# Optimization experiments

Measured on AMD Instinct MI355X. Metric: run time of the kernel, lower is better.

## Reference

```python
import jax, jax.numpy as jnp
import numpy as np

H = 16          # num_heads
K = 15          # kernel_size (padding_l = K-1, causal)
EPS = 1e-5      # LayerNorm eps


def setup_inputs() -> dict:
    key = jax.random.key(0)
    ks = jax.random.split(key, 8)
    T, B, C, F = 1024, 8, 1024, 4096
    n = lambda k, shape, scale=1.0: jax.random.normal(k, shape, jnp.float32) * scale
    return {
        "x": n(ks[0], (T, B, C)),
        "w_lin": n(ks[1], (C, H * K), 0.02),      # dynamic-conv weight projection
        "b_lin": jnp.zeros((H * K,), jnp.float32),
        "ln_g": jnp.ones((C,), jnp.float32),
        "ln_b": jnp.zeros((C,), jnp.float32),
        "fc1_w": n(ks[2], (C, F), 0.02),
        "fc1_b": jnp.zeros((F,), jnp.float32),
        "fc2_w": n(ks[3], (F, C), 0.02),
        "fc2_b": jnp.zeros((C,), jnp.float32),
    }


def _dynamic_conv(x, w_lin, b_lin):
    # x: (T, B, C). Per-timestep weights -> softmax over kernel -> causal conv.
    T, B, C = x.shape
    R = C // H  # channels per head
    w = jnp.einsum('tbc,ck->tbk', x, w_lin) + b_lin          # (T, B, H*K)
    w = jax.nn.softmax(w.reshape(T, B, H, K), axis=-1)        # softmax over kernel taps
    # causal left-padding: tap k sees x[t + k - (K-1)]
    xp = jnp.pad(x, ((K - 1, 0), (0, 0), (0, 0))).reshape(T + K - 1, B, H, R)
    o = jnp.zeros((T, B, H, R), x.dtype)
    for k in range(K):  # fixed small kernel loop; avoids (T,B,C,K) unfold tensor
        o = o + w[:, :, :, k:k + 1] * xp[k:k + T]
    return o.reshape(T, B, C)


def _layer_norm(y, g, b):
    mu = jnp.mean(y, axis=-1, keepdims=True)
    var = jnp.var(y, axis=-1, keepdims=True)
    return (y - mu) * jax.lax.rsqrt(var + EPS) * g + b


def _forward(x, w_lin, b_lin, ln_g, ln_b, fc1_w, fc1_b, fc2_w, fc2_b):
    y = _dynamic_conv(x, w_lin, b_lin)
    y = _layer_norm(y, ln_g, ln_b)
    h = jax.nn.relu(jnp.einsum('tbc,cf->tbf', y, fc1_w) + fc1_b)
    out = jnp.einsum('tbf,fc->tbc', h, fc2_w) + fc2_b
    return out + y  # residual around FFN (residual taken post-LayerNorm)


def reference(x, w_lin, b_lin, ln_g, ln_b, fc1_w, fc1_b, fc2_w, fc2_b):
    return _forward(x, w_lin, b_lin, ln_g, ln_b, fc1_w, fc1_b, fc2_w, fc2_b)
```

## Files before the change

kernel.cpp:

```cpp
#include <hip/hip_runtime.h>


#define T_DIM 1024
#define B_DIM 8
#define C_DIM 1024
#define F_DIM 4096
#define H_DIM 16
#define K_TAP 15
#define TB (T_DIM * B_DIM)

typedef __attribute__((ext_vector_type(8))) short short8;
typedef __attribute__((ext_vector_type(4))) float f32x4;

__device__ __forceinline__ float bf2f(unsigned short u) {
    union { unsigned int i; float f; } v; v.i = ((unsigned int)u) << 16; return v.f;
}
__device__ __forceinline__ unsigned short f2bf(float f) {
    union { float f; unsigned int i; } v; v.f = f;
    unsigned int r = v.i + 0x7fffu + ((v.i >> 16) & 1u);
    return (unsigned short)(r >> 16);
}

__device__ __forceinline__ void async_copy16(const void* gptr, void* lptr) {
    __builtin_amdgcn_global_load_lds(
        (const __attribute__((address_space(1))) void*)gptr,
        (__attribute__((address_space(3))) void*)lptr, 16, 0, 0);
}

__global__ __launch_bounds__(256)
void prep(const float* __restrict__ fc1_w, unsigned short* __restrict__ fc1T,
          const float* __restrict__ fc2_w, unsigned short* __restrict__ fc2T,
          const float* __restrict__ w_lin, unsigned short* __restrict__ wlinT) {
    const int bid = blockIdx.x;
    const int tid = threadIdx.x;
    const float* in; unsigned short* out; int R, Cin, c0, r0;
    if (bid < 1024) {
        int idx = bid;
        in = fc1_w; out = fc1T; R = C_DIM; Cin = F_DIM;
        c0 = (idx & 63) * 64; r0 = (idx >> 6) * 64;
    } else if (bid < 2048) {
        int idx = bid - 1024;
        in = fc2_w; out = fc2T; R = F_DIM; Cin = C_DIM;
        c0 = (idx & 15) * 64; r0 = (idx >> 4) * 64;
    } else {
        int idx = bid - 2048;
        in = w_lin; out = wlinT; R = C_DIM; Cin = 240;
        c0 = (idx & 3) * 64; r0 = (idx >> 2) * 64;
    }
    __shared__ unsigned short tile[64][65];
    const int xx = tid & 63, yy = tid >> 6;
#pragma unroll
    for (int j = 0; j < 16; j++) {
        int r = r0 + yy + j * 4, c = c0 + xx;
        unsigned short v = 0;
        if (c < Cin) v = f2bf(in[(size_t)r * Cin + c]);
        tile[yy + j * 4][xx] = v;
    }
    __syncthreads();
#pragma unroll
    for (int j = 0; j < 16; j++) {
        out[(size_t)(c0 + yy + j * 4) * R + (r0 + xx)] = tile[xx][yy + j * 4];
    }
}

template <int MODE, int SWAP>
__global__ __launch_bounds__(256)
void gemm_bt(const unsigned short* __restrict__ A,
             const unsigned short* __restrict__ Bt,
             void* __restrict__ Cout_v,
             int M, int N, int K, int kz,
             const float* __restrict__ bias,
             const unsigned short* __restrict__ resid) {
    __shared__ __align__(16) unsigned short As[2][128 * 64];
    __shared__ __align__(16) unsigned short Bs[2][128 * 64];

    const int tid = threadIdx.x;
    const int m0 = (SWAP ? blockIdx.x : blockIdx.y) * 128;
    const int n0 = (SWAP ? blockIdx.y : blockIdx.x) * 128;
    const int kbase = blockIdx.z * kz;
    const int wave = tid >> 6, lane = tid & 63;
    const int quad = lane >> 4, l16 = lane & 15;
    const int wm = (wave >> 1) * 64;
    const int wn = (wave & 1) * 64;

    f32x4 acc[4][4];
#pragma unroll
    for (int i = 0; i < 4; i++)
#pragma unroll
        for (int j = 0; j < 4; j++) acc[i][j] = (f32x4){0.f, 0.f, 0.f, 0.f};

    const int rsub = lane >> 3;
    const int gch = (lane & 7) ^ rsub;
    const unsigned short* gA = A + (size_t)(m0 + wave * 32 + rsub) * K + kbase + gch * 8;
    const unsigned short* gB = Bt + (size_t)(n0 + wave * 32 + rsub) * K + kbase + gch * 8;
    unsigned short* lA[2] = {&As[0][wave * 32 * 64], &As[1][wave * 32 * 64]};
    unsigned short* lB[2] = {&Bs[0][wave * 32 * 64], &Bs[1][wave * 32 * 64]};

#pragma unroll
    for (int j = 0; j < 4; j++) {
        async_copy16(gA + (size_t)j * 8 * K, lA[0] + j * 8 * 64);
        async_copy16(gB + (size_t)j * 8 * K, lB[0] + j * 8 * 64);
    }

    const int swz = l16 & 7;
    int buf = 0;
    for (int k0 = 0; k0 < kz; k0 += 64) {
        __syncthreads();

        const int nk = k0 + 64;
        if (nk < kz) {
            const int nb = buf ^ 1;
#pragma unroll
            for (int j = 0; j < 4; j++) {
                async_copy16(gA + nk + (size_t)j * 8 * K, lA[nb] + j * 8 * 64);
                async_copy16(gB + nk + (size_t)j * 8 * K, lB[nb] + j * 8 * 64);
            }
        }

        short8 af[2][4], bfr[2][4];
#pragma unroll
        for (int kk = 0; kk < 2; kk++) {
            const int c = kk * 4 + quad;
#pragma unroll
            for (int i = 0; i < 4; i++) {
                af[kk][i]  = *(const short8*)(&As[buf][(wm + i * 16 + l16) * 64 + (c ^ swz) * 8]);
                bfr[kk][i] = *(const short8*)(&Bs[buf][(wn + i * 16 + l16) * 64 + (c ^ swz) * 8]);
            }
        }
#pragma unroll
        for (int kk = 0; kk < 2; kk++)
#pragma unroll
            for (int mi = 0; mi < 4; mi++)
#pragma unroll
                for (int nj = 0; nj < 4; nj++)
                    acc[mi][nj] = __builtin_amdgcn_mfma_f32_16x16x32_bf16(
                        af[kk][mi], bfr[kk][nj], acc[mi][nj], 0, 0, 0);
        buf ^= 1;
    }

    const int crow0 = m0 + wm + quad * 4;
    const int ccol0 = n0 + wn + l16;
    if (MODE == 1) {
        unsigned short* Cb = (unsigned short*)Cout_v;
        float bv[4];
#pragma unroll
        for (int nj = 0; nj < 4; nj++) bv[nj] = bias[ccol0 + nj * 16];
#pragma unroll
        for (int mi = 0; mi < 4; mi++)
#pragma unroll
            for (int i = 0; i < 4; i++) {
                int rr = crow0 + mi * 16 + i;
#pragma unroll
                for (int nj = 0; nj < 4; nj++) {
                    float v = fmaxf(acc[mi][nj][i] + bv[nj], 0.f);
                    Cb[(size_t)rr * N + ccol0 + nj * 16] = f2bf(v);
                }
            }
    } else {
        float* Cf = (float*)Cout_v;
        float bv[4];
#pragma unroll
        for (int nj = 0; nj < 4; nj++) bv[nj] = bias[ccol0 + nj * 16];
#pragma unroll
        for (int mi = 0; mi < 4; mi++)
#pragma unroll
            for (int i = 0; i < 4; i++) {
                int rr = crow0 + mi * 16 + i;
#pragma unroll
                for (int nj = 0; nj < 4; nj++) {
                    float v = acc[mi][nj][i] + bv[nj]
                            + bf2f(resid[(size_t)rr * N + ccol0 + nj * 16]);
                    Cf[(size_t)rr * N + ccol0 + nj * 16] = v;
                }
            }
    }
}

#define XSP 1032
__global__ __launch_bounds__(256)
void megaconv(const float* __restrict__ x,
              const unsigned short* __restrict__ wlinT,
              const float* __restrict__ b_lin,
              const float* __restrict__ ln_g,
              const float* __restrict__ ln_b,
              unsigned short* __restrict__ y) {
    __shared__ __align__(16) unsigned short xs[30 * XSP];
    __shared__ float wls[16 * 240];
    const int blk = blockIdx.x;
    const int b = blk & 7;
    const int t0 = (blk >> 3) * 16;
    const int tid = threadIdx.x;
    const int wave = tid >> 6, lane = tid & 63;
    const int quad = lane >> 4, l16 = lane & 15;

#pragma unroll
    for (int j = 0; j < 30; j++) {
        const int t = t0 + j - 14;
        uint2 o = make_uint2(0u, 0u);
        if (t >= 0) {
            float4 v = *(const float4*)(x + ((size_t)t * B_DIM + b) * C_DIM + tid * 4);
            o.x = (unsigned int)f2bf(v.x) | ((unsigned int)f2bf(v.y) << 16);
            o.y = (unsigned int)f2bf(v.z) | ((unsigned int)f2bf(v.w) << 16);
        }
        *(uint2*)(&xs[j * XSP + tid * 4]) = o;
    }
    __syncthreads();

    {
        f32x4 lacc[4];
#pragma unroll
        for (int i = 0; i < 4; i++) lacc[i] = (f32x4){0.f, 0.f, 0.f, 0.f};
        const unsigned short* xrow = &xs[(14 + l16) * XSP + quad * 8];
        const unsigned short* brow = wlinT + (size_t)l16 * C_DIM + quad * 8;
#pragma unroll 8
        for (int kk = 0; kk < 32; kk++) {
            short8 af = *(const short8*)(xrow + kk * 32);
#pragma unroll
            for (int j = 0; j < 4; j++) {
                const int nt = wave + j * 4;
                if (nt < 15) {
                    short8 bf = *(const short8*)(brow + (size_t)nt * 16 * C_DIM + kk * 32);
                    lacc[j] = __builtin_amdgcn_mfma_f32_16x16x32_bf16(af, bf, lacc[j], 0, 0, 0);
                }
            }
        }
#pragma unroll
        for (int j = 0; j < 4; j++) {
            const int nt = wave + j * 4;
            if (nt < 15) {
#pragma unroll
                for (int i = 0; i < 4; i++)
                    wls[(quad * 4 + i) * 240 + nt * 16 + l16] = lacc[j][i];
            }
        }
    }
    __syncthreads();

    {
        const int row = tid >> 4, hh = tid & 15;
        float v[K_TAP], mx = -1e30f;
#pragma unroll
        for (int k = 0; k < K_TAP; k++) {
            v[k] = wls[row * 240 + hh * K_TAP + k] + b_lin[hh * K_TAP + k];
            mx = fmaxf(mx, v[k]);
        }
        float s = 0.f;
#pragma unroll
        for (int k = 0; k < K_TAP; k++) { v[k] = __expf(v[k] - mx); s += v[k]; }
        float inv = 1.0f / s;
#pragma unroll
        for (int k = 0; k < K_TAP; k++) wls[row * 240 + hh * K_TAP + k] = v[k] * inv;
    }
    __syncthreads();

    const int chA = lane * 8;
    const int chB = 512 + lane * 8;
    const int hA = lane >> 3;
    const int hB = 8 + (lane >> 3);
    for (int rj = wave; rj < 16; rj += 4) {
        float o[16];
#pragma unroll
        for (int i = 0; i < 16; i++) o[i] = 0.f;
#pragma unroll
        for (int k = 0; k < K_TAP; k++) {
            float wA = wls[rj * 240 + hA * K_TAP + k];
            float wB = wls[rj * 240 + hB * K_TAP + k];
            const unsigned short* xr = &xs[(rj + k) * XSP];
            uint4 pA = *(const uint4*)(xr + chA);
            uint4 pB = *(const uint4*)(xr + chB);
            unsigned int ua[4] = {pA.x, pA.y, pA.z, pA.w};
            unsigned int ub[4] = {pB.x, pB.y, pB.z, pB.w};
#pragma unroll
            for (int q = 0; q < 4; q++) {
                o[2 * q]     += wA * bf2f((unsigned short)(ua[q] & 0xffff));
                o[2 * q + 1] += wA * bf2f((unsigned short)(ua[q] >> 16));
                o[8 + 2 * q]     += wB * bf2f((unsigned short)(ub[q] & 0xffff));
                o[8 + 2 * q + 1] += wB * bf2f((unsigned short)(ub[q] >> 16));
            }
        }
        float s = 0.f, s2 = 0.f;
#pragma unroll
        for (int i = 0; i < 16; i++) { s += o[i]; s2 += o[i] * o[i]; }
#pragma unroll
        for (int off = 32; off > 0; off >>= 1) {
            s  += __shfl_xor(s, off, 64);
            s2 += __shfl_xor(s2, off, 64);
        }
        float mu = s * (1.0f / C_DIM);
        float var = s2 * (1.0f / C_DIM) - mu * mu;
        float rs = rsqrtf(var + 1e-5f);

        unsigned short o16[16];
#pragma unroll
        for (int i = 0; i < 8; i++)
            o16[i] = f2bf((o[i] - mu) * rs * ln_g[chA + i] + ln_b[chA + i]);
#pragma unroll
        for (int i = 0; i < 8; i++)
            o16[8 + i] = f2bf((o[8 + i] - mu) * rs * ln_g[chB + i] + ln_b[chB + i]);
        uint4 w0, w1;
        w0.x = (unsigned int)o16[0]  | ((unsigned int)o16[1]  << 16);
        w0.y = (unsigned int)o16[2]  | ((unsigned int)o16[3]  << 16);
        w0.z = (unsigned int)o16[4]  | ((unsigned int)o16[5]  << 16);
        w0.w = (unsigned int)o16[6]  | ((unsigned int)o16[7]  << 16);
        w1.x = (unsigned int)o16[8]  | ((unsigned int)o16[9]  << 16);
        w1.y = (unsigned int)o16[10] | ((unsigned int)o16[11] << 16);
        w1.z = (unsigned int)o16[12] | ((unsigned int)o16[13] << 16);
        w1.w = (unsigned int)o16[14] | ((unsigned int)o16[15] << 16);
        unsigned short* yr = y + ((size_t)(t0 + rj) * B_DIM + b) * C_DIM;
        *(uint4*)(yr + chA) = w0;
        *(uint4*)(yr + chB) = w1;
    }
}

extern "C" void kernel_launch(void* const* d_in, const int* in_sizes, int n_in,
                              void* d_out, int out_size, void* d_ws, size_t ws_size,
                              hipStream_t stream) {
    const float* x     = (const float*)d_in[0];
    const float* w_lin = (const float*)d_in[1];
    const float* b_lin = (const float*)d_in[2];
    const float* ln_g  = (const float*)d_in[3];
    const float* ln_b  = (const float*)d_in[4];
    const float* fc1_w = (const float*)d_in[5];
    const float* fc1_b = (const float*)d_in[6];
    const float* fc2_w = (const float*)d_in[7];
    const float* fc2_b = (const float*)d_in[8];
    float* out = (float*)d_out;

    char* ws = (char*)d_ws;
    unsigned short* fc1T  = (unsigned short*)(ws + 16777216);
    unsigned short* fc2T  = (unsigned short*)(ws + 25165824);
    unsigned short* wlinT = (unsigned short*)(ws + 33554432);
    unsigned short* y     = (unsigned short*)(ws + 34078720);
    unsigned short* h     = (unsigned short*)(ws + 50855936);

    prep<<<2112, 256, 0, stream>>>(fc1_w, fc1T, fc2_w, fc2T, w_lin, wlinT);

    megaconv<<<TB / 16, 256, 0, stream>>>(x, wlinT, b_lin, ln_g, ln_b, y);

    gemm_bt<1, 0><<<dim3(F_DIM / 128, TB / 128, 1), 256, 0, stream>>>(
        y, fc1T, (void*)h, TB, F_DIM, C_DIM, C_DIM, fc1_b, nullptr);

    gemm_bt<2, 1><<<dim3(TB / 128, C_DIM / 128, 1), 256, 0, stream>>>(
        h, fc2T, (void*)out, TB, C_DIM, F_DIM, F_DIM, fc2_b, y);
}
```

Measured before the change: 359.0 us.

## Split dynamic-conv weight projection into separate split-K tiled GEMM kernel

The per-timestep weight projection (x times w_lin) moves out of the fused conv kernel into a dedicated 128x128 tiled MFMA GEMM. That GEMM reads fp32 x directly, converts it to bf16 while staging into LDS, and splits K in two, writing partial scores to workspace. The conv/LayerNorm kernel then sums the two partials and adds the bias before the softmax. This replaces the old per-block projection, which re-read wlinT from global memory without LDS reuse for every 16-row block. The cost is an extra launch and a round trip of fp32 scores through global memory. The score buffer aliases h, which is safe because the scores are consumed before fc1 writes h.

```diff
diff --git a/kernel.cpp b/kernel.cpp
--- a/kernel.cpp
+++ b/kernel.cpp
@@ -176,14 +176,115 @@
     }
 }
 
+__global__ __launch_bounds__(256)
+void gemm_a32(const float* __restrict__ A32,
+              const unsigned short* __restrict__ Bt,
+              float* __restrict__ Cout,
+              int M, int N, int K, int kz) {
+    __shared__ __align__(16) unsigned short As[2][128 * 64];
+    __shared__ __align__(16) unsigned short Bs[2][128 * 64];
+
+    const int tid = threadIdx.x;
+    const int m0 = blockIdx.y * 128;
+    const int n0 = blockIdx.x * 128;
+    const int kbase = blockIdx.z * kz;
+    const int wave = tid >> 6, lane = tid & 63;
+    const int quad = lane >> 4, l16 = lane & 15;
+    const int wm = (wave >> 1) * 64;
+    const int wn = (wave & 1) * 64;
+
+    f32x4 acc[4][4];
+#pragma unroll
+    for (int i = 0; i < 4; i++)
+#pragma unroll
+        for (int j = 0; j < 4; j++) acc[i][j] = (f32x4){0.f, 0.f, 0.f, 0.f};
+
+    const int ar = tid >> 1, ah = tid & 1;
+    const float* gAf = A32 + (size_t)(m0 + ar) * K + kbase + ah * 32;
+
+    const int rsub = lane >> 3;
+    const int gch = (lane & 7) ^ rsub;
+    const unsigned short* gB = Bt + (size_t)(n0 + wave * 32 + rsub) * K + kbase + gch * 8;
+    unsigned short* lB[2] = {&Bs[0][wave * 32 * 64], &Bs[1][wave * 32 * 64]};
+
+    auto stageA = [&](int k0, int bb) {
+#pragma unroll
+        for (int c = 0; c < 4; c++) {
+            float4 a = *(const float4*)(gAf + k0 + c * 8);
+            float4 b = *(const float4*)(gAf + k0 + c * 8 + 4);
+            uint4 o;
+            o.x = (unsigned int)f2bf(a.x) | ((unsigned int)f2bf(a.y) << 16);
+            o.y = (unsigned int)f2bf(a.z) | ((unsigned int)f2bf(a.w) << 16);
+            o.z = (unsigned int)f2bf(b.x) | ((unsigned int)f2bf(b.y) << 16);
+            o.w = (unsigned int)f2bf(b.z) | ((unsigned int)f2bf(b.w) << 16);
+            const int gc = ah * 4 + c;
+            *(uint4*)(&As[bb][ar * 64 + ((gc ^ (ar & 7)) * 8)]) = o;
+        }
+    };
+
+    stageA(0, 0);
+#pragma unroll
+    for (int j = 0; j < 4; j++)
+        async_copy16(gB + (size_t)j * 8 * K, lB[0] + j * 8 * 64);
+
+    const int swz = l16 & 7;
+    int buf = 0;
+    for (int k0 = 0; k0 < kz; k0 += 64) {
+        __syncthreads();
+
+        const int nk = k0 + 64;
+        if (nk < kz) {
+            const int nb = buf ^ 1;
+            stageA(nk, nb);
+#pragma unroll
+            for (int j = 0; j < 4; j++)
+                async_copy16(gB + nk + (size_t)j * 8 * K, lB[nb] + j * 8 * 64);
+        }
+
+        short8 af[2][4], bfr[2][4];
+#pragma unroll
+        for (int kk = 0; kk < 2; kk++) {
+            const int c = kk * 4 + quad;
+#pragma unroll
+            for (int i = 0; i < 4; i++) {
+                af[kk][i]  = *(const short8*)(&As[buf][(wm + i * 16 + l16) * 64 + (c ^ swz) * 8]);
+                bfr[kk][i] = *(const short8*)(&Bs[buf][(wn + i * 16 + l16) * 64 + (c ^ swz) * 8]);
+            }
+        }
+#pragma unroll
+        for (int kk = 0; kk < 2; kk++)
+#pragma unroll
+            for (int mi = 0; mi < 4; mi++)
+#pragma unroll
+                for (int nj = 0; nj < 4; nj++)
+                    acc[mi][nj] = __builtin_amdgcn_mfma_f32_16x16x32_bf16(
+                        af[kk][mi], bfr[kk][nj], acc[mi][nj], 0, 0, 0);
+        buf ^= 1;
+    }
+
+    float* Cf = Cout + (size_t)blockIdx.z * M * N;
+    const int crow0 = m0 + wm + quad * 4;
+    const int ccol0 = n0 + wn + l16;
+#pragma unroll
+    for (int mi = 0; mi < 4; mi++)
+#pragma unroll
+        for (int i = 0; i < 4; i++) {
+            int rr = crow0 + mi * 16 + i;
+#pragma unroll
+            for (int nj = 0; nj < 4; nj++)
+                Cf[(size_t)rr * N + ccol0 + nj * 16] = acc[mi][nj][i];
+        }
+}
+
 #define XSP 1032
+#define WS_STRIDE ((size_t)TB * 256)
 __global__ __launch_bounds__(256)
-void megaconv(const float* __restrict__ x,
-              const unsigned short* __restrict__ wlinT,
-              const float* __restrict__ b_lin,
-              const float* __restrict__ ln_g,
-              const float* __restrict__ ln_b,
-              unsigned short* __restrict__ y) {
+void conv_ln16s(const float* __restrict__ x,
+                const float* __restrict__ wscore,
+                const float* __restrict__ b_lin,
+                const float* __restrict__ ln_g,
+                const float* __restrict__ ln_b,
+                unsigned short* __restrict__ y) {
     __shared__ __align__(16) unsigned short xs[30 * XSP];
     __shared__ float wls[16 * 240];
     const int blk = blockIdx.x;
@@ -191,7 +292,6 @@
     const int t0 = (blk >> 3) * 16;
     const int tid = threadIdx.x;
     const int wave = tid >> 6, lane = tid & 63;
-    const int quad = lane >> 4, l16 = lane & 15;
 
 #pragma unroll
     for (int j = 0; j < 30; j++) {
@@ -204,44 +304,15 @@
         }
         *(uint2*)(&xs[j * XSP + tid * 4]) = o;
     }
-    __syncthreads();
-
-    {
-        f32x4 lacc[4];
-#pragma unroll
-        for (int i = 0; i < 4; i++) lacc[i] = (f32x4){0.f, 0.f, 0.f, 0.f};
-        const unsigned short* xrow = &xs[(14 + l16) * XSP + quad * 8];
-        const unsigned short* brow = wlinT + (size_t)l16 * C_DIM + quad * 8;
-#pragma unroll 8
-        for (int kk = 0; kk < 32; kk++) {
-            short8 af = *(const short8*)(xrow + kk * 32);
-#pragma unroll
-            for (int j = 0; j < 4; j++) {
-                const int nt = wave + j * 4;
-                if (nt < 15) {
-                    short8 bf = *(const short8*)(brow + (size_t)nt * 16 * C_DIM + kk * 32);
-                    lacc[j] = __builtin_amdgcn_mfma_f32_16x16x32_bf16(af, bf, lacc[j], 0, 0, 0);
-                }
-            }
-        }
-#pragma unroll
-        for (int j = 0; j < 4; j++) {
-            const int nt = wave + j * 4;
-            if (nt < 15) {
-#pragma unroll
-                for (int i = 0; i < 4; i++)
-                    wls[(quad * 4 + i) * 240 + nt * 16 + l16] = lacc[j][i];
-            }
-        }
-    }
-    __syncthreads();
 
     {
         const int row = tid >> 4, hh = tid & 15;
+        const size_t grow = (size_t)(t0 + row) * B_DIM + b;
+        const float* p = wscore + grow * 256 + hh * K_TAP;
         float v[K_TAP], mx = -1e30f;
 #pragma unroll
         for (int k = 0; k < K_TAP; k++) {
-            v[k] = wls[row * 240 + hh * K_TAP + k] + b_lin[hh * K_TAP + k];
+            v[k] = p[k] + p[k + WS_STRIDE] + b_lin[hh * K_TAP + k];
             mx = fmaxf(mx, v[k]);
         }
         float s = 0.f;
@@ -327,15 +398,19 @@
     float* out = (float*)d_out;
 
     char* ws = (char*)d_ws;
-    unsigned short* fc1T  = (unsigned short*)(ws + 16777216);
-    unsigned short* fc2T  = (unsigned short*)(ws + 25165824);
-    unsigned short* wlinT = (unsigned short*)(ws + 33554432);
-    unsigned short* y     = (unsigned short*)(ws + 34078720);
-    unsigned short* h     = (unsigned short*)(ws + 50855936);
+    unsigned short* fc1T  = (unsigned short*)(ws);
+    unsigned short* fc2T  = (unsigned short*)(ws + 8388608);
+    unsigned short* wlinT = (unsigned short*)(ws + 16777216);
+    unsigned short* y     = (unsigned short*)(ws + 17301504);
+    unsigned short* h     = (unsigned short*)(ws + 34078720);
+    float* wscore = (float*)(ws + 34078720);
 
     prep<<<2112, 256, 0, stream>>>(fc1_w, fc1T, fc2_w, fc2T, w_lin, wlinT);
 
-    megaconv<<<TB / 16, 256, 0, stream>>>(x, wlinT, b_lin, ln_g, ln_b, y);
+    gemm_a32<<<dim3(256 / 128, TB / 128, 2), 256, 0, stream>>>(
+        x, wlinT, wscore, TB, 256, C_DIM, C_DIM / 2);
+
+    conv_ln16s<<<TB / 16, 256, 0, stream>>>(x, wscore, b_lin, ln_g, ln_b, y);
 
     gemm_bt<1, 0><<<dim3(F_DIM / 128, TB / 128, 1), 256, 0, stream>>>(
         y, fc1T, (void*)h, TB, F_DIM, C_DIM, C_DIM, fc1_b, nullptr);
```

Result: faster. 305.9 us (-14.8%).
